# Kernel tuning notes

Measured on AMD Instinct MI355X. Metric: run time of the kernel, lower is better.

Reference implementation:

```python
import jax, jax.numpy as jnp
import numpy as np

NUM_NODES = 100000
NUM_HYPEREDGES = 20000
NUM_SEMALINKS = 5000
NUM_EDGES = 600000
IN_DIM = 128
SIGNAL_DIM = 64
OUT_DIM = 128


def setup_inputs() -> dict:
    key = jax.random.key(0)
    k = jax.random.split(key, 8)
    node_embeddings = jax.random.normal(k[0], (NUM_NODES, IN_DIM), dtype=jnp.float32)
    semalink_embeddings = jax.random.normal(k[1], (NUM_SEMALINKS, SIGNAL_DIM), dtype=jnp.float32)
    hyperedge_embeddings = jax.random.normal(k[2], (NUM_HYPEREDGES, IN_DIM), dtype=jnp.float32)
    node_idx = jax.random.randint(k[3], (NUM_EDGES,), 0, NUM_NODES, dtype=jnp.int32)
    sl_idx = jax.random.randint(k[4], (NUM_EDGES,), 0, NUM_SEMALINKS, dtype=jnp.int32)
    he_idx = jax.random.randint(k[5], (NUM_EDGES,), 0, NUM_HYPEREDGES, dtype=jnp.int32)
    semalinks = jnp.stack([node_idx, sl_idx, he_idx], axis=1)  # [E, 3]
    W_a = jax.random.normal(k[6], (IN_DIM, SIGNAL_DIM), dtype=jnp.float32)
    W_f = jax.random.normal(k[7], (2 * IN_DIM, OUT_DIM), dtype=jnp.float32)
    return {
        'node_embeddings': node_embeddings,
        'semalink_embeddings': semalink_embeddings,
        'hyperedge_embeddings': hyperedge_embeddings,
        'semalinks': semalinks,
        'W_a': W_a,
        'W_f': W_f,
    }


def reference(node_embeddings, semalink_embeddings, hyperedge_embeddings, semalinks, W_a, W_f):
    # Original loops edges in order, ASSIGNING final_embeddings[node_idx] each time:
    # only the LAST edge touching each node determines that node's output.
    E = semalinks.shape[0]
    n_idx = semalinks[:, 0]
    s_idx = semalinks[:, 1]
    h_idx = semalinks[:, 2]

    order = jnp.arange(E, dtype=jnp.int32)
    last = jax.ops.segment_max(order, n_idx, num_segments=NUM_NODES)  # [N]
    has_edge = last >= 0
    last_c = jnp.clip(last, 0, E - 1)

    sel_h = h_idx[last_c]  # [N]
    sel_s = s_idx[last_c]  # [N]
    h_emb = hyperedge_embeddings[sel_h]          # [N, in_dim]
    sl_emb = semalink_embeddings[sel_s]          # [N, signal_dim]

    # per-node attention score (1x1 in original)
    r_h = node_embeddings @ W_a                  # [N, signal_dim]
    r_t = h_emb @ W_a                            # [N, signal_dim]
    score = jnp.sum(r_h * jnp.tanh(r_t + sl_emb), axis=-1, keepdims=True)  # [N, 1]
    gamma = jax.nn.softmax(score, axis=-1)       # softmax over singleton == 1.0 (same as torch)
    f = gamma * h_emb                            # [N, in_dim]

    u = jnp.concatenate([f, node_embeddings], axis=-1) @ W_f  # [N, out_dim]
    out = jnp.where(has_edge[:, None], u, jnp.zeros((), dtype=u.dtype))
    return out
```

## Files before the change

kernel.cpp:

```cpp
#include <hip/hip_runtime.h>
#include <hip/hip_bf16.h>

#define NNODES 100000
#define NHE 20000
#define NEDGES 600000

typedef float f32x4 __attribute__((ext_vector_type(4)));
typedef short bf16x8 __attribute__((ext_vector_type(8)));
typedef short bf16x4 __attribute__((ext_vector_type(4)));

__device__ __forceinline__ unsigned short f2bf(float f) {
    unsigned u = __builtin_bit_cast(unsigned, f);
    u += 0x7fffu + ((u >> 16) & 1u);
    return (unsigned short)(u >> 16);
}

__global__ void k_setup(int* __restrict__ last, const float* __restrict__ Wf,
                        unsigned short* __restrict__ wt) {
    int b = blockIdx.x, t = threadIdx.x;
    if (b < 391) {
        int i = b * 256 + t;
        if (i < NNODES) last[i] = -1;
    } else {
        int idx = (b - 391) * 256 + t;
        int k = idx >> 7, c = idx & 127;
        wt[c * 256 + k] = f2bf(Wf[idx]);
    }
}

__global__ void k_scatter(const int* __restrict__ sl, int* __restrict__ last) {
    int e = blockIdx.x * 256 + threadIdx.x;
    if (e < NEDGES) atomicMax(&last[sl[3 * e]], e);
}

__global__ __launch_bounds__(256) void k_main(
    const float* __restrict__ node_emb,
    const float* __restrict__ he_emb,
    const int* __restrict__ sl,
    const int* __restrict__ last,
    const unsigned short* __restrict__ wt,
    float* __restrict__ out)
{
    __shared__ __align__(16) unsigned short Xs[2][64 * 64];
    __shared__ int he_s[64];
    __shared__ int valid_s[64];

    int t = threadIdx.x;
    int r0 = blockIdx.x * 64;

    if (t < 64) {
        int ri = r0 + t;
        int e = (ri < NNODES) ? last[ri] : -1;
        int v = (e >= 0) ? 1 : 0;
        valid_s[t] = v;
        he_s[t] = v ? sl[3 * e + 2] : 0;
    }
    __syncthreads();

    int lane = t & 63, w = t >> 6;
    int wm = w >> 1, wn = w & 1;
    int l15 = lane & 15, l4 = lane >> 4;
    int tr = t >> 4, q = t & 15;

    f32x4 acc[2][4] = {};
    f32x4 pre[4];

    #pragma unroll
    for (int i = 0; i < 4; ++i) {
        int row = i * 16 + tr;
        pre[i] = *(const f32x4*)(he_emb + he_s[row] * 128 + q * 4);
    }

    #pragma unroll
    for (int kc = 0; kc < 4; ++kc) {
        #pragma unroll
        for (int i = 0; i < 4; ++i) {
            int row = i * 16 + tr;
            bf16x4 p;
            p[0] = (short)f2bf(pre[i][0]);
            p[1] = (short)f2bf(pre[i][1]);
            p[2] = (short)f2bf(pre[i][2]);
            p[3] = (short)f2bf(pre[i][3]);
            int byte = (row * 128 + q * 8) ^ ((row & 7) << 4);
            *(bf16x4*)((char*)Xs[kc & 1] + byte) = p;
        }
        if (kc < 3) {
            int kn = kc + 1;
            #pragma unroll
            for (int i = 0; i < 4; ++i) {
                int row = i * 16 + tr;
                const float* s;
                if (kn < 2) {
                    s = he_emb + he_s[row] * 128 + kn * 64 + q * 4;
                } else {
                    int ri = r0 + row;
                    if (ri >= NNODES) ri = NNODES - 1;
                    s = node_emb + ri * 128 + (kn - 2) * 64 + q * 4;
                }
                pre[i] = *(const f32x4*)s;
            }
        }
        asm volatile("s_waitcnt lgkmcnt(0)" ::: "memory");
        __builtin_amdgcn_sched_barrier(0);
        __builtin_amdgcn_s_barrier();
        __builtin_amdgcn_sched_barrier(0);

        #pragma unroll
        for (int ks = 0; ks < 2; ++ks) {
            bf16x8 a[2], b[4];
            #pragma unroll
            for (int fm = 0; fm < 2; ++fm) {
                int row = wm * 32 + fm * 16 + l15;
                int byte = (row * 128 + ks * 64 + l4 * 16) ^ ((row & 7) << 4);
                a[fm] = *(const bf16x8*)((const char*)Xs[kc & 1] + byte);
            }
            #pragma unroll
            for (int fn = 0; fn < 4; ++fn) {
                int col = wn * 64 + fn * 16 + l15;
                b[fn] = *(const bf16x8*)(wt + col * 256 + kc * 64 + ks * 32 + l4 * 8);
            }
            #pragma unroll
            for (int fm = 0; fm < 2; ++fm)
                #pragma unroll
                for (int fn = 0; fn < 4; ++fn)
                    acc[fm][fn] = __builtin_amdgcn_mfma_f32_16x16x32_bf16(
                        a[fm], b[fn], acc[fm][fn], 0, 0, 0);
        }
    }

    #pragma unroll
    for (int fm = 0; fm < 2; ++fm) {
        #pragma unroll
        for (int j = 0; j < 4; ++j) {
            int lrow = wm * 32 + fm * 16 + l4 * 4 + j;
            int ri = r0 + lrow;
            if (ri < NNODES) {
                int v = valid_s[lrow];
                #pragma unroll
                for (int fn = 0; fn < 4; ++fn) {
                    int col = wn * 64 + fn * 16 + l15;
                    out[ri * 128 + col] = v ? acc[fm][fn][j] : 0.0f;
                }
            }
        }
    }
}

extern "C" void kernel_launch(void* const* d_in, const int* in_sizes, int n_in,
                              void* d_out, int out_size, void* d_ws, size_t ws_size,
                              hipStream_t stream) {
    const float* node_emb = (const float*)d_in[0];
    const float* he_emb = (const float*)d_in[2];
    const int* sl = (const int*)d_in[3];
    const float* Wf = (const float*)d_in[5];
    float* out = (float*)d_out;

    int* last = (int*)d_ws;
    unsigned short* wt = (unsigned short*)((char*)d_ws + 400128);

    k_setup<<<519, 256, 0, stream>>>(last, Wf, wt);
    k_scatter<<<(NEDGES + 255) / 256, 256, 0, stream>>>(sl, last);
    k_main<<<(NNODES + 63) / 64, 256, 0, stream>>>(node_emb, he_emb, sl, last, wt, out);
}
```

Before: 78.37 us.

## Drop LDS staging, load A fragments straight to registers, fuse setup kernels

The main kernel no longer stages the gathered hyperedge and node rows through shared memory with barriers. Each wave now owns 16 rows, loads its own A fragments from global memory straight into registers, converts them to bf16 and issues MFMAs across all 128 output columns. The weight transpose is folded into the scatter kernel, and the init of the last-edge array becomes a hipMemsetAsync, removing one kernel launch. In exchange, each wave now reads all B weights (8 fragments per k-step) from global or L2 where it used to read 4.

Measured after the change: 103.8 us. +32.5%, slower.

```diff
diff --git a/kernel.cpp b/kernel.cpp
--- a/kernel.cpp
+++ b/kernel.cpp
@@ -7,7 +7,6 @@
 
 typedef float f32x4 __attribute__((ext_vector_type(4)));
 typedef short bf16x8 __attribute__((ext_vector_type(8)));
-typedef short bf16x4 __attribute__((ext_vector_type(4)));
 
 __device__ __forceinline__ unsigned short f2bf(float f) {
     unsigned u = __builtin_bit_cast(unsigned, f);
@@ -15,22 +14,26 @@
     return (unsigned short)(u >> 16);
 }
 
-__global__ void k_setup(int* __restrict__ last, const float* __restrict__ Wf,
-                        unsigned short* __restrict__ wt) {
+__device__ __forceinline__ bf16x8 cvt8(f32x4 a, f32x4 b) {
+    bf16x8 r;
+    r[0] = (short)f2bf(a[0]); r[1] = (short)f2bf(a[1]);
+    r[2] = (short)f2bf(a[2]); r[3] = (short)f2bf(a[3]);
+    r[4] = (short)f2bf(b[0]); r[5] = (short)f2bf(b[1]);
+    r[6] = (short)f2bf(b[2]); r[7] = (short)f2bf(b[3]);
+    return r;
+}
+
+__global__ void k_scatter(const int* __restrict__ sl, int* __restrict__ last,
+                          const float* __restrict__ Wf, unsigned short* __restrict__ wt) {
     int b = blockIdx.x, t = threadIdx.x;
-    if (b < 391) {
-        int i = b * 256 + t;
-        if (i < NNODES) last[i] = -1;
+    if (b < 2344) {
+        int e = b * 256 + t;
+        if (e < NEDGES) atomicMax(&last[sl[3 * e]], e);
     } else {
-        int idx = (b - 391) * 256 + t;
+        int idx = (b - 2344) * 256 + t;
         int k = idx >> 7, c = idx & 127;
         wt[c * 256 + k] = f2bf(Wf[idx]);
     }
-}
-
-__global__ void k_scatter(const int* __restrict__ sl, int* __restrict__ last) {
-    int e = blockIdx.x * 256 + threadIdx.x;
-    if (e < NEDGES) atomicMax(&last[sl[3 * e]], e);
 }
 
 __global__ __launch_bounds__(256) void k_main(
@@ -41,7 +44,6 @@
     const unsigned short* __restrict__ wt,
     float* __restrict__ out)
 {
-    __shared__ __align__(16) unsigned short Xs[2][64 * 64];
     __shared__ int he_s[64];
     __shared__ int valid_s[64];
 
@@ -51,97 +53,60 @@
     if (t < 64) {
         int ri = r0 + t;
         int e = (ri < NNODES) ? last[ri] : -1;
-        int v = (e >= 0) ? 1 : 0;
-        valid_s[t] = v;
-        he_s[t] = v ? sl[3 * e + 2] : 0;
+        valid_s[t] = (e >= 0) ? 1 : 0;
+        he_s[t] = (e >= 0) ? sl[3 * e + 2] : 0;
     }
     __syncthreads();
 
     int lane = t & 63, w = t >> 6;
-    int wm = w >> 1, wn = w & 1;
     int l15 = lane & 15, l4 = lane >> 4;
-    int tr = t >> 4, q = t & 15;
+    int rw = r0 + w * 16;
 
-    f32x4 acc[2][4] = {};
-    f32x4 pre[4];
+    int hr = he_s[w * 16 + l15];
+    int nr = rw + l15; if (nr >= NNODES) nr = NNODES - 1;
+    const float* hp = he_emb + (long)hr * 128 + l4 * 8;
+    const float* np = node_emb + (long)nr * 128 + l4 * 8;
+    const unsigned short* wp = wt + (long)l15 * 256 + l4 * 8;
 
-    #pragma unroll
-    for (int i = 0; i < 4; ++i) {
-        int row = i * 16 + tr;
-        pre[i] = *(const f32x4*)(he_emb + he_s[row] * 128 + q * 4);
-    }
+    f32x4 acc[8] = {};
+    f32x4 A[2][4];
+
+    A[0][0] = *(const f32x4*)(hp + 0);
+    A[0][1] = *(const f32x4*)(hp + 4);
+    A[0][2] = *(const f32x4*)(hp + 32);
+    A[0][3] = *(const f32x4*)(hp + 36);
 
     #pragma unroll
     for (int kc = 0; kc < 4; ++kc) {
-        #pragma unroll
-        for (int i = 0; i < 4; ++i) {
-            int row = i * 16 + tr;
-            bf16x4 p;
-            p[0] = (short)f2bf(pre[i][0]);
-            p[1] = (short)f2bf(pre[i][1]);
-            p[2] = (short)f2bf(pre[i][2]);
-            p[3] = (short)f2bf(pre[i][3]);
-            int byte = (row * 128 + q * 8) ^ ((row & 7) << 4);
-            *(bf16x4*)((char*)Xs[kc & 1] + byte) = p;
+        if (kc < 3) {
+            const float* s = (kc + 1 < 2) ? (hp + (kc + 1) * 64) : (np + (kc - 1) * 64);
+            A[(kc + 1) & 1][0] = *(const f32x4*)(s + 0);
+            A[(kc + 1) & 1][1] = *(const f32x4*)(s + 4);
+            A[(kc + 1) & 1][2] = *(const f32x4*)(s + 32);
+            A[(kc + 1) & 1][3] = *(const f32x4*)(s + 36);
         }
-        if (kc < 3) {
-            int kn = kc + 1;
-            #pragma unroll
-            for (int i = 0; i < 4; ++i) {
-                int row = i * 16 + tr;
-                const float* s;
-                if (kn < 2) {
-                    s = he_emb + he_s[row] * 128 + kn * 64 + q * 4;
-                } else {
-                    int ri = r0 + row;
-                    if (ri >= NNODES) ri = NNODES - 1;
-                    s = node_emb + ri * 128 + (kn - 2) * 64 + q * 4;
-                }
-                pre[i] = *(const f32x4*)s;
-            }
-        }
-        asm volatile("s_waitcnt lgkmcnt(0)" ::: "memory");
-        __builtin_amdgcn_sched_barrier(0);
-        __builtin_amdgcn_s_barrier();
-        __builtin_amdgcn_sched_barrier(0);
-
         #pragma unroll
         for (int ks = 0; ks < 2; ++ks) {
-            bf16x8 a[2], b[4];
+            bf16x8 a = cvt8(A[kc & 1][ks * 2], A[kc & 1][ks * 2 + 1]);
+            bf16x8 bw[8];
             #pragma unroll
-            for (int fm = 0; fm < 2; ++fm) {
-                int row = wm * 32 + fm * 16 + l15;
-                int byte = (row * 128 + ks * 64 + l4 * 16) ^ ((row & 7) << 4);
-                a[fm] = *(const bf16x8*)((const char*)Xs[kc & 1] + byte);
-            }
+            for (int fn = 0; fn < 8; ++fn)
+                bw[fn] = *(const bf16x8*)(wp + fn * 4096 + kc * 64 + ks * 32);
             #pragma unroll
-            for (int fn = 0; fn < 4; ++fn) {
-                int col = wn * 64 + fn * 16 + l15;
-                b[fn] = *(const bf16x8*)(wt + col * 256 + kc * 64 + ks * 32 + l4 * 8);
-            }
-            #pragma unroll
-            for (int fm = 0; fm < 2; ++fm)
-                #pragma unroll
-                for (int fn = 0; fn < 4; ++fn)
-                    acc[fm][fn] = __builtin_amdgcn_mfma_f32_16x16x32_bf16(
-                        a[fm], b[fn], acc[fm][fn], 0, 0, 0);
+            for (int fn = 0; fn < 8; ++fn)
+                acc[fn] = __builtin_amdgcn_mfma_f32_16x16x32_bf16(a, bw[fn], acc[fn], 0, 0, 0);
         }
     }
 
     #pragma unroll
-    for (int fm = 0; fm < 2; ++fm) {
-        #pragma unroll
-        for (int j = 0; j < 4; ++j) {
-            int lrow = wm * 32 + fm * 16 + l4 * 4 + j;
-            int ri = r0 + lrow;
-            if (ri < NNODES) {
-                int v = valid_s[lrow];
-                #pragma unroll
-                for (int fn = 0; fn < 4; ++fn) {
-                    int col = wn * 64 + fn * 16 + l15;
-                    out[ri * 128 + col] = v ? acc[fm][fn][j] : 0.0f;
-                }
-            }
+    for (int j = 0; j < 4; ++j) {
+        int row = l4 * 4 + j;
+        int ri = rw + row;
+        if (ri < NNODES) {
+            int v = valid_s[w * 16 + row];
+            #pragma unroll
+            for (int fn = 0; fn < 8; ++fn)
+                out[(long)ri * 128 + fn * 16 + l15] = v ? acc[fn][j] : 0.0f;
         }
     }
 }
@@ -158,7 +123,7 @@
     int* last = (int*)d_ws;
     unsigned short* wt = (unsigned short*)((char*)d_ws + 400128);
 
-    k_setup<<<519, 256, 0, stream>>>(last, Wf, wt);
-    k_scatter<<<(NEDGES + 255) / 256, 256, 0, stream>>>(sl, last);
+    hipMemsetAsync(last, 0xFF, NNODES * sizeof(int), stream);
+    k_scatter<<<2344 + 128, 256, 0, stream>>>(sl, last, Wf, wt);
     k_main<<<(NNODES + 63) / 64, 256, 0, stream>>>(node_emb, he_emb, sl, last, wt, out);
 }
```

## Precompute hyperedge projection once per hyperedge and gather projected rows

Applied to the files above, without the earlier changes.

Uses linearity of the final matmul: h_emb @ W_f[:128] is computed once per hyperedge (20k rows) in a new kernel and stored as bf16, and the main kernel only multiplies node embeddings by the lower half of W_f before adding the gathered projected row. This roughly halves the main GEMM's K dimension and replaces the random fp32 gathers of 128-wide hyperedge rows with bf16 gathers in the epilogue. The last-index init moves to a memset and the scatter is merged with the weight transpose. It adds an extra kernel launch and an extra bf16 rounding of the hyperedge product, and it drops the software-pipelined double buffering in the main kernel.

New measurement: 90.15 us. 1.15x slower.

```diff
diff --git a/kernel.cpp b/kernel.cpp
--- a/kernel.cpp
+++ b/kernel.cpp
@@ -14,34 +14,100 @@
     u += 0x7fffu + ((u >> 16) & 1u);
     return (unsigned short)(u >> 16);
 }
-
-__global__ void k_setup(int* __restrict__ last, const float* __restrict__ Wf,
-                        unsigned short* __restrict__ wt) {
+__device__ __forceinline__ float bf2f(unsigned short h) {
+    unsigned u = ((unsigned)h) << 16;
+    return __builtin_bit_cast(float, u);
+}
+
+__global__ void k_sc(const int* __restrict__ sl, int* __restrict__ last,
+                     const float* __restrict__ Wf, unsigned short* __restrict__ wt) {
     int b = blockIdx.x, t = threadIdx.x;
-    if (b < 391) {
-        int i = b * 256 + t;
-        if (i < NNODES) last[i] = -1;
+    if (b < 2344) {
+        int e = b * 256 + t;
+        if (e < NEDGES) atomicMax(&last[sl[3 * e]], e);
     } else {
-        int idx = (b - 391) * 256 + t;
+        int idx = (b - 2344) * 256 + t;
         int k = idx >> 7, c = idx & 127;
         wt[c * 256 + k] = f2bf(Wf[idx]);
     }
 }
 
-__global__ void k_scatter(const int* __restrict__ sl, int* __restrict__ last) {
-    int e = blockIdx.x * 256 + threadIdx.x;
-    if (e < NEDGES) atomicMax(&last[sl[3 * e]], e);
+__global__ __launch_bounds__(256) void k_he(
+    const float* __restrict__ he_emb,
+    const unsigned short* __restrict__ wt,
+    unsigned short* __restrict__ heo)
+{
+    __shared__ __align__(16) unsigned short Xs[64 * 128];
+    int t = threadIdx.x;
+    int r0 = blockIdx.x * 64;
+
+    #pragma unroll
+    for (int i = 0; i < 8; ++i) {
+        int idx = i * 256 + t;
+        int row = idx >> 5, q = idx & 31;
+        int ri = r0 + row; if (ri >= NHE) ri = NHE - 1;
+        f32x4 v = *(const f32x4*)(he_emb + (long)ri * 128 + q * 4);
+        bf16x4 p;
+        p[0] = (short)f2bf(v[0]); p[1] = (short)f2bf(v[1]);
+        p[2] = (short)f2bf(v[2]); p[3] = (short)f2bf(v[3]);
+        int byte = (row * 256 + q * 8) ^ ((row & 7) << 4);
+        *(bf16x4*)((char*)Xs + byte) = p;
+    }
+    __syncthreads();
+
+    int lane = t & 63, w = t >> 6;
+    int wm = w >> 1, wn = w & 1;
+    int l15 = lane & 15, l4 = lane >> 4;
+
+    f32x4 acc[2][4] = {};
+    #pragma unroll
+    for (int kc = 0; kc < 2; ++kc)
+        #pragma unroll
+        for (int ks = 0; ks < 2; ++ks) {
+            bf16x8 a[2], b[4];
+            #pragma unroll
+            for (int fm = 0; fm < 2; ++fm) {
+                int row = wm * 32 + fm * 16 + l15;
+                int byte = (row * 256 + kc * 128 + ks * 64 + l4 * 16) ^ ((row & 7) << 4);
+                a[fm] = *(const bf16x8*)((const char*)Xs + byte);
+            }
+            #pragma unroll
+            for (int fn = 0; fn < 4; ++fn) {
+                int col = wn * 64 + fn * 16 + l15;
+                b[fn] = *(const bf16x8*)(wt + (long)col * 256 + kc * 64 + ks * 32 + l4 * 8);
+            }
+            #pragma unroll
+            for (int fm = 0; fm < 2; ++fm)
+                #pragma unroll
+                for (int fn = 0; fn < 4; ++fn)
+                    acc[fm][fn] = __builtin_amdgcn_mfma_f32_16x16x32_bf16(
+                        a[fm], b[fn], acc[fm][fn], 0, 0, 0);
+        }
+
+    #pragma unroll
+    for (int fm = 0; fm < 2; ++fm)
+        #pragma unroll
+        for (int j = 0; j < 4; ++j) {
+            int ri = r0 + wm * 32 + fm * 16 + l4 * 4 + j;
+            if (ri < NHE) {
+                #pragma unroll
+                for (int fn = 0; fn < 4; ++fn) {
+                    int col = wn * 64 + fn * 16 + l15;
+                    heo[(long)ri * 128 + col] = f2bf(acc[fm][fn][j]);
+                }
+            }
+        }
 }
 
 __global__ __launch_bounds__(256) void k_main(
     const float* __restrict__ node_emb,
-    const float* __restrict__ he_emb,
     const int* __restrict__ sl,
     const int* __restrict__ last,
     const unsigned short* __restrict__ wt,
+    const unsigned short* __restrict__ heo,
     float* __restrict__ out)
 {
-    __shared__ __align__(16) unsigned short Xs[2][64 * 64];
+    __shared__ __align__(16) unsigned short Xs[64 * 128];
     __shared__ int he_s[64];
     __shared__ int valid_s[64];
 
@@ -51,73 +117,44 @@
     if (t < 64) {
         int ri = r0 + t;
         int e = (ri < NNODES) ? last[ri] : -1;
-        int v = (e >= 0) ? 1 : 0;
-        valid_s[t] = v;
-        he_s[t] = v ? sl[3 * e + 2] : 0;
+        valid_s[t] = (e >= 0) ? 1 : 0;
+        he_s[t] = (e >= 0) ? sl[3 * e + 2] : 0;
+    }
+
+    #pragma unroll
+    for (int i = 0; i < 8; ++i) {
+        int idx = i * 256 + t;
+        int row = idx >> 5, q = idx & 31;
+        int ri = r0 + row; if (ri >= NNODES) ri = NNODES - 1;
+        f32x4 v = *(const f32x4*)(node_emb + (long)ri * 128 + q * 4);
+        bf16x4 p;
+        p[0] = (short)f2bf(v[0]); p[1] = (short)f2bf(v[1]);
+        p[2] = (short)f2bf(v[2]); p[3] = (short)f2bf(v[3]);
+        int byte = (row * 256 + q * 8) ^ ((row & 7) << 4);
+        *(bf16x4*)((char*)Xs + byte) = p;
     }
     __syncthreads();
 
     int lane = t & 63, w = t >> 6;
     int wm = w >> 1, wn = w & 1;
     int l15 = lane & 15, l4 = lane >> 4;
-    int tr = t >> 4, q = t & 15;
 
     f32x4 acc[2][4] = {};
-    f32x4 pre[4];
-
-    #pragma unroll
-    for (int i = 0; i < 4; ++i) {
-        int row = i * 16 + tr;
-        pre[i] = *(const f32x4*)(he_emb + he_s[row] * 128 + q * 4);
-    }
-
-    #pragma unroll
-    for (int kc = 0; kc < 4; ++kc) {
-        #pragma unroll
-        for (int i = 0; i < 4; ++i) {
-            int row = i * 16 + tr;
-            bf16x4 p;
-            p[0] = (short)f2bf(pre[i][0]);
-            p[1] = (short)f2bf(pre[i][1]);
-            p[2] = (short)f2bf(pre[i][2]);
-            p[3] = (short)f2bf(pre[i][3]);
-            int byte = (row * 128 + q * 8) ^ ((row & 7) << 4);
-            *(bf16x4*)((char*)Xs[kc & 1] + byte) = p;
-        }
-        if (kc < 3) {
-            int kn = kc + 1;
-            #pragma unroll
-            for (int i = 0; i < 4; ++i) {
-                int row = i * 16 + tr;
-                const float* s;
-                if (kn < 2) {
-                    s = he_emb + he_s[row] * 128 + kn * 64 + q * 4;
-                } else {
-                    int ri = r0 + row;
-                    if (ri >= NNODES) ri = NNODES - 1;
-                    s = node_emb + ri * 128 + (kn - 2) * 64 + q * 4;
-                }
-                pre[i] = *(const f32x4*)s;
-            }
-        }
-        asm volatile("s_waitcnt lgkmcnt(0)" ::: "memory");
-        __builtin_amdgcn_sched_barrier(0);
-        __builtin_amdgcn_s_barrier();
-        __builtin_amdgcn_sched_barrier(0);
-
+    #pragma unroll
+    for (int kc = 0; kc < 2; ++kc)
         #pragma unroll
         for (int ks = 0; ks < 2; ++ks) {
             bf16x8 a[2], b[4];
             #pragma unroll
             for (int fm = 0; fm < 2; ++fm) {
                 int row = wm * 32 + fm * 16 + l15;
-                int byte = (row * 128 + ks * 64 + l4 * 16) ^ ((row & 7) << 4);
-                a[fm] = *(const bf16x8*)((const char*)Xs[kc & 1] + byte);
+                int byte = (row * 256 + kc * 128 + ks * 64 + l4 * 16) ^ ((row & 7) << 4);
+                a[fm] = *(const bf16x8*)((const char*)Xs + byte);
             }
             #pragma unroll
             for (int fn = 0; fn < 4; ++fn) {
                 int col = wn * 64 + fn * 16 + l15;
-                b[fn] = *(const bf16x8*)(wt + col * 256 + kc * 64 + ks * 32 + l4 * 8);
+                b[fn] = *(const bf16x8*)(wt + (long)col * 256 + 128 + kc * 64 + ks * 32 + l4 * 8);
             }
             #pragma unroll
             for (int fm = 0; fm < 2; ++fm)
@@ -126,24 +163,24 @@
                     acc[fm][fn] = __builtin_amdgcn_mfma_f32_16x16x32_bf16(
                         a[fm], b[fn], acc[fm][fn], 0, 0, 0);
         }
-    }
-
-    #pragma unroll
-    for (int fm = 0; fm < 2; ++fm) {
+
+    #pragma unroll
+    for (int fm = 0; fm < 2; ++fm)
         #pragma unroll
         for (int j = 0; j < 4; ++j) {
             int lrow = wm * 32 + fm * 16 + l4 * 4 + j;
             int ri = r0 + lrow;
             if (ri < NNODES) {
                 int v = valid_s[lrow];
+                int hr = he_s[lrow];
                 #pragma unroll
                 for (int fn = 0; fn < 4; ++fn) {
                     int col = wn * 64 + fn * 16 + l15;
-                    out[ri * 128 + col] = v ? acc[fm][fn][j] : 0.0f;
+                    float hv = bf2f(heo[(long)hr * 128 + col]);
+                    out[(long)ri * 128 + col] = v ? (acc[fm][fn][j] + hv) : 0.0f;
                 }
             }
         }
-    }
 }
 
 extern "C" void kernel_launch(void* const* d_in, const int* in_sizes, int n_in,
@@ -157,8 +194,10 @@
 
     int* last = (int*)d_ws;
     unsigned short* wt = (unsigned short*)((char*)d_ws + 400128);
-
-    k_setup<<<519, 256, 0, stream>>>(last, Wf, wt);
-    k_scatter<<<(NEDGES + 255) / 256, 256, 0, stream>>>(sl, last);
-    k_main<<<(NNODES + 63) / 64, 256, 0, stream>>>(node_emb, he_emb, sl, last, wt, out);
-}
+    unsigned short* heo = (unsigned short*)((char*)d_ws + 465664);
+
+    hipMemsetAsync(last, 0xFF, NNODES * sizeof(int), stream);
+    k_sc<<<2344 + 128, 256, 0, stream>>>(sl, last, Wf, wt);
+    k_he<<<(NHE + 63) / 64, 256, 0, stream>>>(he_emb, wt, heo);
+    k_main<<<(NNODES + 63) / 64, 256, 0, stream>>>(node_emb, sl, last, wt, heo, out);
+}
```
